# Optimization experiments

Hardware: AMD Instinct MI355X
Metric: run time of the kernel (lower is better)

Reference implementation:

```python
import jax, jax.numpy as jnp
import numpy as np

IN, OUT, HID = 256, 256, 512
BATCH, T = 16, 4096


def setup_inputs() -> dict:
    key = jax.random.key(0)
    ks = jax.random.split(key, 10)
    # nu/theta init as in the original module (r_min=0, r_max=1)
    u1 = jax.random.uniform(ks[0], (HID,))
    nu = -0.5 * jnp.log(u1)  # uniform in (0,1) -> nu > 0
    nu_log = jnp.log(nu)
    theta = (jnp.pi / 10.0) * jax.random.uniform(ks[1], (HID,))
    theta_log = jnp.log(theta)
    # glorot-uniform style scales
    sB = float(np.sqrt(6.0 / (HID + IN)))
    sC = float(np.sqrt(6.0 / (OUT + HID)))
    sD = float(np.sqrt(6.0 / (OUT + IN)))
    B_re = jax.random.uniform(ks[2], (HID, IN), minval=-sB, maxval=sB)
    B_im = jax.random.uniform(ks[3], (HID, IN), minval=-sB, maxval=sB)
    C_re = jax.random.uniform(ks[4], (OUT, HID), minval=-sC, maxval=sC)
    C_im = jax.random.uniform(ks[5], (OUT, HID), minval=-sC, maxval=sC)
    D = jax.random.uniform(ks[6], (OUT, IN), minval=-sD, maxval=sD)
    bh_re = jnp.zeros((HID,), jnp.float32)
    bh_im = jnp.zeros((HID,), jnp.float32)
    bias_output = jnp.zeros((OUT,), jnp.float32)
    X = jax.random.normal(ks[7], (BATCH, T, IN), dtype=jnp.float32)
    return {
        "X": X, "nu_log": nu_log, "theta_log": theta_log,
        "B_re": B_re, "B_im": B_im, "C_re": C_re, "C_im": C_im,
        "D": D, "bh_re": bh_re, "bh_im": bh_im, "bias_output": bias_output,
    }


def reference(X, nu_log, theta_log, B_re, B_im, C_re, C_im, D, bh_re, bh_im, bias_output):
    # lambda = exp(-exp(nu_log) + i*exp(theta_log));  |lambda| = exp(-exp(nu_log))
    mag = jnp.exp(-jnp.exp(nu_log))                       # [H], real
    lam = mag * jnp.exp(1j * jnp.exp(theta_log))          # [H], complex64
    gamma = jnp.sqrt(1.0 - mag * mag)                     # [H], real
    B = B_re + 1j * B_im                                  # [H, I]
    C = C_re + 1j * C_im                                  # [O, H]
    bias_h = bh_re + 1j * bh_im                           # [H]
    # input drive precomputed for all timesteps: gamma * (B @ x_t) + bias_hidden
    Bu = jnp.einsum("bti,hi->bth", X.astype(jnp.complex64), B)  # [B,T,H]
    drive = gamma.astype(jnp.complex64) * Bu + bias_h           # [B,T,H]

    def step(h, d_t):  # h: [B,H] complex, d_t: [B,H] complex
        h = lam * h + d_t
        return h, h

    h0 = jnp.zeros((X.shape[0], lam.shape[0]), jnp.complex64)
    _, H = jax.lax.scan(step, h0, jnp.swapaxes(drive, 0, 1))  # H: [T,B,H]
    H = jnp.swapaxes(H, 0, 1)                                 # [B,T,H]
    Y = (jnp.real(jnp.einsum("bth,oh->bto", H, C))
         + jnp.einsum("bti,oi->bto", X, D)
         + bias_output)
    return Y
```

## Files before the change

### kernel.cpp

```cpp
#include <hip/hip_runtime.h>
#include <hip/hip_bf16.h>


#define TT     4096
#define BATCHN 16
#define MM     (BATCHN * TT)
#define LCH    64
#define NCH    (TT / LCH)

typedef unsigned short u16;
typedef short bf16x8 __attribute__((ext_vector_type(8)));
typedef float f32x4 __attribute__((ext_vector_type(4)));

__device__ __forceinline__ u16 f2bf(float f) {
  union { __hip_bfloat16 b; u16 u; } cv;
  cv.b = __float2bfloat16(f);
  return cv.u;
}
__device__ __forceinline__ float bf2f(u16 u) {
  union { u16 u; __hip_bfloat16 b; } cv;
  cv.u = u;
  return __bfloat162float(cv.b);
}

__global__ void k_params(const float* __restrict__ nu_log,
                         const float* __restrict__ theta_log,
                         float* __restrict__ P) {
  int h = threadIdx.x;
  if (h >= 512) return;
  double nu  = exp((double)nu_log[h]);
  double th  = exp((double)theta_log[h]);
  double mag = exp(-nu);
  double g   = sqrt(fmax(0.0, 1.0 - mag * mag));
  double magL = exp(-(double)LCH * nu);
  double aL   = (double)LCH * th;
  P[h]        = (float)(mag * cos(th));
  P[512 + h]  = (float)(mag * sin(th));
  P[1024 + h] = (float)g;
  P[1536 + h] = (float)(magL * cos(aL));
  P[2048 + h] = (float)(magL * sin(aL));
}

__global__ void k_prep_w(const float* __restrict__ Bre, const float* __restrict__ Bim,
                         const float* __restrict__ Cre, const float* __restrict__ Cim,
                         const float* __restrict__ D, u16* __restrict__ Bcat,
                         u16* __restrict__ Ccat) {
  const int NB = 1024 * 256;
  const int NC = 256 * 1280;
  for (int idx = blockIdx.x * blockDim.x + threadIdx.x; idx < NB + NC;
       idx += gridDim.x * blockDim.x) {
    if (idx < NB) {
      int row = idx >> 8, col = idx & 255;
      float v = (row < 512) ? Bre[row * 256 + col] : Bim[(row - 512) * 256 + col];
      Bcat[idx] = f2bf(v);
    } else {
      int j = idx - NB;
      int row = j / 1280, col = j % 1280;
      float v;
      if (col < 512)       v =  Cre[row * 512 + col];
      else if (col < 1024) v = -Cim[row * 512 + (col - 512)];
      else                 v =  D[row * 256 + (col - 1024)];
      Ccat[j] = f2bf(v);
    }
  }
}

__global__ __launch_bounds__(256) void k_prep_x(const float* __restrict__ X,
                                                u16* __restrict__ Xb) {
  int idx = blockIdx.x * 256 + threadIdx.x;
  const float4* s = (const float4*)X + (size_t)idx * 2;
  float4 a = s[0], b = s[1];
  u16 o[8] = {f2bf(a.x), f2bf(a.y), f2bf(a.z), f2bf(a.w),
              f2bf(b.x), f2bf(b.y), f2bf(b.z), f2bf(b.w)};
  *(int4*)(Xb + (size_t)idx * 8) = *(const int4*)o;
}

__global__ __launch_bounds__(256) void k_gemm1(
    const u16* __restrict__ Xb, const u16* __restrict__ Bcat,
    const float* __restrict__ P, const float* __restrict__ bhr,
    const float* __restrict__ bhi, u16* __restrict__ Hbuf) {
  __shared__ __align__(16) char smem[2 * 128 * 64 * 2];
  char* sA = smem;
  char* sB = smem + 128 * 64 * 2;
  const int tid = threadIdx.x;
  const int lane = tid & 63;
  const int wid = tid >> 6;
  const int wr = wid >> 1, wc = wid & 1;
  const int mb = blockIdx.x * 128;
  const int nb = blockIdx.y * 128;

  f32x4 acc[4][4];
#pragma unroll
  for (int r = 0; r < 4; ++r)
#pragma unroll
    for (int c = 0; c < 4; ++c) acc[r][c] = (f32x4)0.f;

  for (int kt = 0; kt < 4; ++kt) {
    const int k0 = kt * 64;
    __syncthreads();
#pragma unroll
    for (int i = 0; i < 4; ++i) {
      int s = i * 256 + tid;
      int row = s >> 3, slot = s & 7;
      int4 va = *(const int4*)(Xb + (size_t)(mb + row) * 256 + k0 + slot * 8);
      int4 vb = *(const int4*)(Bcat + (size_t)(nb + row) * 256 + k0 + slot * 8);
      int soff = row * 128 + ((slot ^ (row & 7)) << 4);
      *(int4*)(sA + soff) = va;
      *(int4*)(sB + soff) = vb;
    }
    __syncthreads();
#pragma unroll
    for (int kk = 0; kk < 2; ++kk) {
      bf16x8 af[4], bfr[4];
#pragma unroll
      for (int r = 0; r < 4; ++r) {
        int row = wr * 64 + r * 16 + (lane & 15);
        int slot = (kk * 4 + (lane >> 4)) ^ (row & 7);
        af[r] = *(const bf16x8*)(sA + row * 128 + slot * 16);
      }
#pragma unroll
      for (int c = 0; c < 4; ++c) {
        int row = wc * 64 + c * 16 + (lane & 15);
        int slot = (kk * 4 + (lane >> 4)) ^ (row & 7);
        bfr[c] = *(const bf16x8*)(sB + row * 128 + slot * 16);
      }
#pragma unroll
      for (int r = 0; r < 4; ++r)
#pragma unroll
        for (int c = 0; c < 4; ++c)
          acc[r][c] = __builtin_amdgcn_mfma_f32_16x16x32_bf16(af[r], bfr[c],
                                                              acc[r][c], 0, 0, 0);
    }
  }
  const int rbase = (lane >> 4) * 4;
  const int cbase = lane & 15;
#pragma unroll
  for (int r = 0; r < 4; ++r)
#pragma unroll
    for (int c = 0; c < 4; ++c) {
      int col = nb + wc * 64 + c * 16 + cbase;
      int h = col & 511;
      float g = P[1024 + h];
      float bias = (col < 512) ? bhr[h] : bhi[h];
#pragma unroll
      for (int q = 0; q < 4; ++q) {
        int row = mb + wr * 64 + r * 16 + rbase + q;
        Hbuf[(size_t)row * 1024 + col] = f2bf(fmaf(acc[r][c][q], g, bias));
      }
    }
}

__global__ __launch_bounds__(512) void k_scanF(
    const float* __restrict__ P, const u16* __restrict__ Hbuf,
    float* __restrict__ finr, float* __restrict__ fini) {
  const int h = threadIdx.x;
  const int b = blockIdx.x, c = blockIdx.y;
  const float lr = P[h], li = P[512 + h];
  float hr = 0.f, hi = 0.f;
  size_t base = ((size_t)b * TT + (size_t)c * LCH) * 1024 + h;
  for (int j = 0; j < LCH; ++j) {
    float dr = bf2f(Hbuf[base]);
    float di = bf2f(Hbuf[base + 512]);
    float nr = fmaf(lr, hr, fmaf(-li, hi, dr));
    float ni = fmaf(lr, hi, fmaf(li, hr, di));
    hr = nr; hi = ni;
    base += 1024;
  }
  size_t f = ((size_t)b * NCH + c) * 512 + h;
  finr[f] = hr; fini[f] = hi;
}

__global__ __launch_bounds__(512) void k_carry(
    const float* __restrict__ P, const float* __restrict__ finr,
    const float* __restrict__ fini, float* __restrict__ carr,
    float* __restrict__ cari) {
  const int h = threadIdx.x;
  const int b = blockIdx.x;
  const float Lr = P[1536 + h], Li = P[2048 + h];
  float cr = 0.f, ci = 0.f;
  for (int c = 0; c < NCH; ++c) {
    size_t idx = ((size_t)b * NCH + c) * 512 + h;
    carr[idx] = cr; cari[idx] = ci;
    float fr = finr[idx], fi = fini[idx];
    float nr = fmaf(Lr, cr, fmaf(-Li, ci, fr));
    float ni = fmaf(Lr, ci, fmaf(Li, cr, fi));
    cr = nr; ci = ni;
  }
}

__global__ __launch_bounds__(512) void k_scanW(
    const float* __restrict__ P, u16* __restrict__ Hbuf,
    const float* __restrict__ carr, const float* __restrict__ cari) {
  const int h = threadIdx.x;
  const int b = blockIdx.x, c = blockIdx.y;
  const float lr = P[h], li = P[512 + h];
  size_t cidx = ((size_t)b * NCH + c) * 512 + h;
  float hr = carr[cidx], hi = cari[cidx];
  size_t base = ((size_t)b * TT + (size_t)c * LCH) * 1024 + h;
  for (int j = 0; j < LCH; ++j) {
    float dr = bf2f(Hbuf[base]);
    float di = bf2f(Hbuf[base + 512]);
    float nr = fmaf(lr, hr, fmaf(-li, hi, dr));
    float ni = fmaf(lr, hi, fmaf(li, hr, di));
    hr = nr; hi = ni;
    Hbuf[base] = f2bf(hr);
    Hbuf[base + 512] = f2bf(hi);
    base += 1024;
  }
}

__global__ __launch_bounds__(256) void k_gemm2(
    const u16* __restrict__ Hbuf, const u16* __restrict__ Xb,
    const u16* __restrict__ Ccat, const float* __restrict__ bo,
    float* __restrict__ Y) {
  __shared__ __align__(16) char smem[2 * 128 * 64 * 2];
  char* sA = smem;
  char* sB = smem + 128 * 64 * 2;
  const int tid = threadIdx.x;
  const int lane = tid & 63;
  const int wid = tid >> 6;
  const int wr = wid >> 1, wc = wid & 1;
  const int mb = blockIdx.x * 128;
  const int nb = blockIdx.y * 128;

  f32x4 acc[4][4];
#pragma unroll
  for (int r = 0; r < 4; ++r)
#pragma unroll
    for (int c = 0; c < 4; ++c) acc[r][c] = (f32x4)0.f;

  for (int kt = 0; kt < 20; ++kt) {
    const int k0 = kt * 64;
    const u16* Asrc;
    size_t lda;
    int ka;
    if (kt < 16) { Asrc = Hbuf; lda = 1024; ka = k0; }
    else         { Asrc = Xb;   lda = 256;  ka = k0 - 1024; }
    __syncthreads();
#pragma unroll
    for (int i = 0; i < 4; ++i) {
      int s = i * 256 + tid;
      int row = s >> 3, slot = s & 7;
      int4 va = *(const int4*)(Asrc + (size_t)(mb + row) * lda + ka + slot * 8);
      int4 vb = *(const int4*)(Ccat + (size_t)(nb + row) * 1280 + k0 + slot * 8);
      int soff = row * 128 + ((slot ^ (row & 7)) << 4);
      *(int4*)(sA + soff) = va;
      *(int4*)(sB + soff) = vb;
    }
    __syncthreads();
#pragma unroll
    for (int kk = 0; kk < 2; ++kk) {
      bf16x8 af[4], bfr[4];
#pragma unroll
      for (int r = 0; r < 4; ++r) {
        int row = wr * 64 + r * 16 + (lane & 15);
        int slot = (kk * 4 + (lane >> 4)) ^ (row & 7);
        af[r] = *(const bf16x8*)(sA + row * 128 + slot * 16);
      }
#pragma unroll
      for (int c = 0; c < 4; ++c) {
        int row = wc * 64 + c * 16 + (lane & 15);
        int slot = (kk * 4 + (lane >> 4)) ^ (row & 7);
        bfr[c] = *(const bf16x8*)(sB + row * 128 + slot * 16);
      }
#pragma unroll
      for (int r = 0; r < 4; ++r)
#pragma unroll
        for (int c = 0; c < 4; ++c)
          acc[r][c] = __builtin_amdgcn_mfma_f32_16x16x32_bf16(af[r], bfr[c],
                                                              acc[r][c], 0, 0, 0);
    }
  }
  const int rbase = (lane >> 4) * 4;
  const int cbase = lane & 15;
#pragma unroll
  for (int r = 0; r < 4; ++r)
#pragma unroll
    for (int c = 0; c < 4; ++c) {
      int col = nb + wc * 64 + c * 16 + cbase;
      float bias = bo[col];
#pragma unroll
      for (int q = 0; q < 4; ++q) {
        int row = mb + wr * 64 + r * 16 + rbase + q;
        Y[(size_t)row * 256 + col] = acc[r][c][q] + bias;
      }
    }
}

extern "C" void kernel_launch(void* const* d_in, const int* in_sizes, int n_in,
                              void* d_out, int out_size, void* d_ws, size_t ws_size,
                              hipStream_t stream) {
  const float* X        = (const float*)d_in[0];
  const float* nu_log   = (const float*)d_in[1];
  const float* theta_lg = (const float*)d_in[2];
  const float* Bre      = (const float*)d_in[3];
  const float* Bim      = (const float*)d_in[4];
  const float* Cre      = (const float*)d_in[5];
  const float* Cim      = (const float*)d_in[6];
  const float* D        = (const float*)d_in[7];
  const float* bhr      = (const float*)d_in[8];
  const float* bhi      = (const float*)d_in[9];
  const float* bo       = (const float*)d_in[10];
  float* Y = (float*)d_out;
  char* ws = (char*)d_ws;

  size_t off = 0;
  float* P = (float*)(ws + off);            off += 2560 * 4;
  off = (off + 255) & ~(size_t)255;
  u16* Hbuf = (u16*)(ws + off);             off += (size_t)MM * 1024 * 2;
  u16* Xb   = (u16*)(ws + off);             off += (size_t)MM * 256 * 2;
  u16* Bcat = (u16*)(ws + off);             off += 1024 * 256 * 2;
  u16* Ccat = (u16*)(ws + off);             off += 256 * 1280 * 2;
  float* finr = (float*)(ws + off);         off += (size_t)BATCHN * NCH * 512 * 4;
  float* fini = (float*)(ws + off);         off += (size_t)BATCHN * NCH * 512 * 4;
  float* carr = (float*)(ws + off);         off += (size_t)BATCHN * NCH * 512 * 4;
  float* cari = (float*)(ws + off);         off += (size_t)BATCHN * NCH * 512 * 4;
  if (ws_size < off) return;

  k_params<<<1, 512, 0, stream>>>(nu_log, theta_lg, P);
  k_prep_w<<<512, 256, 0, stream>>>(Bre, Bim, Cre, Cim, D, Bcat, Ccat);
  k_prep_x<<<MM * 256 / (256 * 8), 256, 0, stream>>>(X, Xb);
  k_gemm1<<<dim3(MM / 128, 8), 256, 0, stream>>>(Xb, Bcat, P, bhr, bhi, Hbuf);
  k_scanF<<<dim3(BATCHN, NCH), 512, 0, stream>>>(P, Hbuf, finr, fini);
  k_carry<<<BATCHN, 512, 0, stream>>>(P, finr, fini, carr, cari);
  k_scanW<<<dim3(BATCHN, NCH), 512, 0, stream>>>(P, Hbuf, carr, cari);
  k_gemm2<<<dim3(MM / 128, 2), 256, 0, stream>>>(Hbuf, Xb, Ccat, bo, Y);
}
```

Baseline: 336.3 us.

## Fuse carry-apply scan with output GEMM via shared-memory hidden tile

Merges the second scan pass and the output GEMM into one kernel: each block scans a 64-step chunk for one batch, writes the bf16 hidden states into a swizzled 64KB LDS tile, and feeds that tile straight into MFMA against Ccat. Ccat is reordered so each 256-wide half of H has its real and imaginary parts contiguous, letting the GEMM run in two K-halves of 512. This drops the global write-back of the scanned states and their re-read by the GEMM. In exchange, B fragments are loaded straight from global memory with no LDS staging, M per block is only 64 rows, and the large LDS footprint limits occupancy. It also adds unroll pragmas on the scan loops.

New measurement: 324.2 us. 1.04x faster.

```diff
diff --git a/kernel.cpp b/kernel.cpp
--- a/kernel.cpp
+++ b/kernel.cpp
@@ -55,11 +55,15 @@
       Bcat[idx] = f2bf(v);
     } else {
       int j = idx - NB;
-      int row = j / 1280, col = j % 1280;
+      int o = j / 1280, k = j % 1280;
       float v;
-      if (col < 512)       v =  Cre[row * 512 + col];
-      else if (col < 1024) v = -Cim[row * 512 + (col - 512)];
-      else                 v =  D[row * 256 + (col - 1024)];
+      if (k < 1024) {
+        int q = k >> 9, kk = k & 511;
+        int h = q * 256 + (kk & 255);
+        v = (kk < 256) ? Cre[o * 512 + h] : -Cim[o * 512 + h];
+      } else {
+        v = D[o * 256 + (k - 1024)];
+      }
       Ccat[j] = f2bf(v);
     }
   }
@@ -158,6 +162,7 @@
   const float lr = P[h], li = P[512 + h];
   float hr = 0.f, hi = 0.f;
   size_t base = ((size_t)b * TT + (size_t)c * LCH) * 1024 + h;
+#pragma unroll 8
   for (int j = 0; j < LCH; ++j) {
     float dr = bf2f(Hbuf[base]);
     float di = bf2f(Hbuf[base + 512]);
@@ -188,101 +193,116 @@
   }
 }
 
-__global__ __launch_bounds__(512) void k_scanW(
-    const float* __restrict__ P, u16* __restrict__ Hbuf,
-    const float* __restrict__ carr, const float* __restrict__ cari) {
-  const int h = threadIdx.x;
-  const int b = blockIdx.x, c = blockIdx.y;
-  const float lr = P[h], li = P[512 + h];
-  size_t cidx = ((size_t)b * NCH + c) * 512 + h;
-  float hr = carr[cidx], hi = cari[cidx];
-  size_t base = ((size_t)b * TT + (size_t)c * LCH) * 1024 + h;
-  for (int j = 0; j < LCH; ++j) {
-    float dr = bf2f(Hbuf[base]);
-    float di = bf2f(Hbuf[base + 512]);
-    float nr = fmaf(lr, hr, fmaf(-li, hi, dr));
-    float ni = fmaf(lr, hi, fmaf(li, hr, di));
-    hr = nr; hi = ni;
-    Hbuf[base] = f2bf(hr);
-    Hbuf[base + 512] = f2bf(hi);
-    base += 1024;
-  }
-}
-
-__global__ __launch_bounds__(256) void k_gemm2(
-    const u16* __restrict__ Hbuf, const u16* __restrict__ Xb,
-    const u16* __restrict__ Ccat, const float* __restrict__ bo,
-    float* __restrict__ Y) {
-  __shared__ __align__(16) char smem[2 * 128 * 64 * 2];
-  char* sA = smem;
-  char* sB = smem + 128 * 64 * 2;
+__global__ __launch_bounds__(256) void k_fused2(
+    const float* __restrict__ P, const u16* __restrict__ Hbuf,
+    const u16* __restrict__ Xb, const u16* __restrict__ Ccat,
+    const float* __restrict__ carr, const float* __restrict__ cari,
+    const float* __restrict__ bo, float* __restrict__ Y) {
+  __shared__ __align__(16) char Hs[64 * 1024];
   const int tid = threadIdx.x;
   const int lane = tid & 63;
-  const int wid = tid >> 6;
-  const int wr = wid >> 1, wc = wid & 1;
-  const int mb = blockIdx.x * 128;
-  const int nb = blockIdx.y * 128;
+  const int w = tid >> 6;
+  const int c = blockIdx.x;
+  const int b = blockIdx.y;
+  const int row0 = b * TT + c * LCH;
 
   f32x4 acc[4][4];
 #pragma unroll
-  for (int r = 0; r < 4; ++r)
-#pragma unroll
-    for (int c = 0; c < 4; ++c) acc[r][c] = (f32x4)0.f;
-
-  for (int kt = 0; kt < 20; ++kt) {
-    const int k0 = kt * 64;
-    const u16* Asrc;
-    size_t lda;
-    int ka;
-    if (kt < 16) { Asrc = Hbuf; lda = 1024; ka = k0; }
-    else         { Asrc = Xb;   lda = 256;  ka = k0 - 1024; }
+  for (int m = 0; m < 4; ++m)
+#pragma unroll
+    for (int n = 0; n < 4; ++n) acc[m][n] = (f32x4)0.f;
+
+#pragma unroll
+  for (int q = 0; q < 2; ++q) {
+    const int h = q * 256 + tid;
+    const float lr = P[h], li = P[512 + h];
+    size_t cidx = ((size_t)b * NCH + c) * 512 + h;
+    float hr = carr[cidx], hi = cari[cidx];
+    size_t base = (size_t)row0 * 1024 + h;
     __syncthreads();
-#pragma unroll
-    for (int i = 0; i < 4; ++i) {
-      int s = i * 256 + tid;
-      int row = s >> 3, slot = s & 7;
-      int4 va = *(const int4*)(Asrc + (size_t)(mb + row) * lda + ka + slot * 8);
-      int4 vb = *(const int4*)(Ccat + (size_t)(nb + row) * 1280 + k0 + slot * 8);
-      int soff = row * 128 + ((slot ^ (row & 7)) << 4);
-      *(int4*)(sA + soff) = va;
-      *(int4*)(sB + soff) = vb;
+#pragma unroll 8
+    for (int j = 0; j < LCH; ++j) {
+      float dr = bf2f(Hbuf[base]);
+      float di = bf2f(Hbuf[base + 512]);
+      float nr = fmaf(lr, hr, fmaf(-li, hi, dr));
+      float ni = fmaf(lr, hi, fmaf(li, hr, di));
+      hr = nr; hi = ni;
+      int sre = ((tid >> 3) ^ (j & 7)) * 16 + (tid & 7) * 2;
+      int sim = (((256 + tid) >> 3) ^ (j & 7)) * 16 + (tid & 7) * 2;
+      *(u16*)(Hs + j * 1024 + sre) = f2bf(nr);
+      *(u16*)(Hs + j * 1024 + sim) = f2bf(ni);
+      base += 1024;
     }
     __syncthreads();
-#pragma unroll
-    for (int kk = 0; kk < 2; ++kk) {
+#pragma unroll 4
+    for (int ks = 0; ks < 16; ++ks) {
       bf16x8 af[4], bfr[4];
 #pragma unroll
-      for (int r = 0; r < 4; ++r) {
-        int row = wr * 64 + r * 16 + (lane & 15);
-        int slot = (kk * 4 + (lane >> 4)) ^ (row & 7);
-        af[r] = *(const bf16x8*)(sA + row * 128 + slot * 16);
-      }
-#pragma unroll
-      for (int c = 0; c < 4; ++c) {
-        int row = wc * 64 + c * 16 + (lane & 15);
-        int slot = (kk * 4 + (lane >> 4)) ^ (row & 7);
-        bfr[c] = *(const bf16x8*)(sB + row * 128 + slot * 16);
-      }
-#pragma unroll
-      for (int r = 0; r < 4; ++r)
-#pragma unroll
-        for (int c = 0; c < 4; ++c)
-          acc[r][c] = __builtin_amdgcn_mfma_f32_16x16x32_bf16(af[r], bfr[c],
-                                                              acc[r][c], 0, 0, 0);
-    }
-  }
-  const int rbase = (lane >> 4) * 4;
-  const int cbase = lane & 15;
-#pragma unroll
-  for (int r = 0; r < 4; ++r)
-#pragma unroll
-    for (int c = 0; c < 4; ++c) {
-      int col = nb + wc * 64 + c * 16 + cbase;
+      for (int m = 0; m < 4; ++m) {
+        int row = m * 16 + (lane & 15);
+        int slot = (ks * 4 + (lane >> 4)) ^ (row & 7);
+        af[m] = *(const bf16x8*)(Hs + row * 1024 + slot * 16);
+      }
+#pragma unroll
+      for (int n = 0; n < 4; ++n) {
+        int col = w * 64 + n * 16 + (lane & 15);
+        bfr[n] = *(const bf16x8*)(Ccat + (size_t)col * 1280 + q * 512 +
+                                  ks * 32 + (lane >> 4) * 8);
+      }
+#pragma unroll
+      for (int m = 0; m < 4; ++m)
+#pragma unroll
+        for (int n = 0; n < 4; ++n)
+          acc[m][n] = __builtin_amdgcn_mfma_f32_16x16x32_bf16(af[m], bfr[n],
+                                                              acc[m][n], 0, 0, 0);
+    }
+  }
+
+  __syncthreads();
+#pragma unroll
+  for (int i = 0; i < 8; ++i) {
+    int p = i * 256 + tid;
+    int row = p >> 5, slot = p & 31;
+    int4 v = *(const int4*)(Xb + (size_t)(row0 + row) * 256 +
+                            ((slot ^ (row & 7)) * 8));
+    *(int4*)(Hs + row * 512 + slot * 16) = v;
+  }
+  __syncthreads();
+#pragma unroll 2
+  for (int ks = 0; ks < 8; ++ks) {
+    bf16x8 af[4], bfr[4];
+#pragma unroll
+    for (int m = 0; m < 4; ++m) {
+      int row = m * 16 + (lane & 15);
+      int slot = (ks * 4 + (lane >> 4)) ^ (row & 7);
+      af[m] = *(const bf16x8*)(Hs + row * 512 + slot * 16);
+    }
+#pragma unroll
+    for (int n = 0; n < 4; ++n) {
+      int col = w * 64 + n * 16 + (lane & 15);
+      bfr[n] = *(const bf16x8*)(Ccat + (size_t)col * 1280 + 1024 +
+                                ks * 32 + (lane >> 4) * 8);
+    }
+#pragma unroll
+    for (int m = 0; m < 4; ++m)
+#pragma unroll
+      for (int n = 0; n < 4; ++n)
+        acc[m][n] = __builtin_amdgcn_mfma_f32_16x16x32_bf16(af[m], bfr[n],
+                                                            acc[m][n], 0, 0, 0);
+  }
+
+  const int rb = (lane >> 4) * 4;
+  const int cb = lane & 15;
+#pragma unroll
+  for (int m = 0; m < 4; ++m)
+#pragma unroll
+    for (int n = 0; n < 4; ++n) {
+      int col = w * 64 + n * 16 + cb;
       float bias = bo[col];
 #pragma unroll
-      for (int q = 0; q < 4; ++q) {
-        int row = mb + wr * 64 + r * 16 + rbase + q;
-        Y[(size_t)row * 256 + col] = acc[r][c][q] + bias;
+      for (int qq = 0; qq < 4; ++qq) {
+        int row = row0 + m * 16 + rb + qq;
+        Y[(size_t)row * 256 + col] = acc[m][n][qq] + bias;
       }
     }
 }
@@ -323,6 +343,6 @@
   k_gemm1<<<dim3(MM / 128, 8), 256, 0, stream>>>(Xb, Bcat, P, bhr, bhi, Hbuf);
   k_scanF<<<dim3(BATCHN, NCH), 512, 0, stream>>>(P, Hbuf, finr, fini);
   k_carry<<<BATCHN, 512, 0, stream>>>(P, finr, fini, carr, cari);
-  k_scanW<<<dim3(BATCHN, NCH), 512, 0, stream>>>(P, Hbuf, carr, cari);
-  k_gemm2<<<dim3(MM / 128, 2), 256, 0, stream>>>(Hbuf, Xb, Ccat, bo, Y);
-}
+  k_fused2<<<dim3(NCH, BATCHN), 256, 0, stream>>>(P, Hbuf, Xb, Ccat, carr, cari,
+                                                  bo, Y);
+}
```
